# Kernel tuning notes

Hardware: AMD Instinct MI355X
Metric: run time of the kernel (lower is better)

## Reference

```python
import jax, jax.numpy as jnp
import numpy as np


def setup_inputs() -> dict:
    key = jax.random.key(0)
    k1, k2 = jax.random.split(key, 2)
    N, H, W, FIN = 64, 64, 64, 64
    FH, FW, FOUT = 4, 4, 128
    L = (H // FH) * (W // FW)  # 256 output locations (stride == kernel)
    X = jax.random.normal(k1, (N, H, W, FIN), dtype=jnp.float32)
    # 'alexnet' init: normal(0, 0.01), unshared per-location filters
    filters = 0.01 * jax.random.normal(k2, (1, L, FH, FW, FIN, FOUT), dtype=jnp.float32)
    bias = jnp.zeros((FOUT,), dtype=jnp.float32)  # bias init value 0.0
    return {"X": X, "filters": filters, "bias": bias}


def reference(X, filters, bias):
    N, H, W, C = X.shape
    _, L, fh, fw, fin, fout = filters.shape
    rows, cols = H // fh, W // fw
    # image_to_patches (stride==kernel branch): non-overlapping patch extraction
    # patches[n, r*cols+c, i, j, ch] = X[n, r*fh+i, c*fw+j, ch]
    patches = X.reshape(N, rows, fh, cols, fw, C)
    patches = patches.transpose(0, 1, 3, 2, 4, 5).reshape(N, L, fh, fw, C)
    # broadcast-multiply + reduce_sum over (fh, fw, fin) == per-location GEMM
    Z = jnp.einsum('nlijc,lijcf->nlf', patches, filters[0]) + bias
    Z = Z.reshape(N, rows, cols, fout)
    return jax.nn.relu(Z)
```

## Files before the change

kernel.cpp:

```cpp
#include <hip/hip_runtime.h>


typedef __bf16 bf16x8 __attribute__((ext_vector_type(8)));
typedef float f32x4 __attribute__((ext_vector_type(4)));

#define SA 72
#define SB 132

__device__ __forceinline__ unsigned short f2bf(float f) {
  unsigned u = __builtin_bit_cast(unsigned, f);
  u += 0x7fffu + ((u >> 16) & 1u);
  return (unsigned short)(u >> 16);
}
__device__ __forceinline__ unsigned pack2(float a, float b) {
  return (unsigned)f2bf(a) | ((unsigned)f2bf(b) << 16);
}

__global__ __launch_bounds__(256) void bioconv_mfma(
    const float* __restrict__ X, const float* __restrict__ Fw,
    const float* __restrict__ bias, float* __restrict__ out) {
  const int l = blockIdx.x;
  const int r = l >> 4;
  const int c = l & 15;
  const int t = threadIdx.x;
  const int w = t >> 6;
  const int lane = t & 63;
  const int q = lane >> 4;
  const int nl = lane & 15;

  __shared__ __align__(16) unsigned short As[2][64 * SA];
  __shared__ __align__(16) unsigned Bs[2][32 * SB];

  const float* Fl = Fw + (size_t)l * 131072;

  f32x4 acc[4][2];
#pragma unroll
  for (int mb = 0; mb < 4; ++mb)
#pragma unroll
    for (int fb = 0; fb < 2; ++fb)
      acc[mb][fb] = (f32x4){0.f, 0.f, 0.f, 0.f};

  float4 areg[4], b0reg[4], b1reg[4];

  const int a_n0 = t >> 4;
  const int a_f4 = t & 15;
  const int b_kp0 = t >> 5;
  const int b_f = (t & 31) << 2;

  const float* xrowbase = X + c * 256 + a_f4 * 4;

  auto issue_loads = [&](int s) {
    const int i = s >> 2;
    const int koff = (s & 3) << 6;
    const float* xb = xrowbase + (r * 4 + i) * 4096 + koff;
#pragma unroll
    for (int rep = 0; rep < 4; ++rep) {
      const int n = a_n0 + (rep << 4);
      areg[rep] = *(const float4*)(xb + (size_t)n * 262144);
    }
    const float* fbse = Fl + s * 8192 + b_f;
#pragma unroll
    for (int rep = 0; rep < 4; ++rep) {
      const int kp = b_kp0 + (rep << 3);
      const float* g = fbse + kp * 256;
      b0reg[rep] = *(const float4*)(g);
      b1reg[rep] = *(const float4*)(g + 128);
    }
  };

  auto store_lds = [&](int buf) {
#pragma unroll
    for (int rep = 0; rep < 4; ++rep) {
      const int n = a_n0 + (rep << 4);
      uint2 v;
      v.x = pack2(areg[rep].x, areg[rep].y);
      v.y = pack2(areg[rep].z, areg[rep].w);
      *(uint2*)&As[buf][n * SA + a_f4 * 4] = v;
    }
#pragma unroll
    for (int rep = 0; rep < 4; ++rep) {
      const int kp = b_kp0 + (rep << 3);
      uint4 v;
      v.x = pack2(b0reg[rep].x, b1reg[rep].x);
      v.y = pack2(b0reg[rep].y, b1reg[rep].y);
      v.z = pack2(b0reg[rep].z, b1reg[rep].z);
      v.w = pack2(b0reg[rep].w, b1reg[rep].w);
      *(uint4*)&Bs[buf][kp * SB + b_f] = v;
    }
  };

  issue_loads(0);
  store_lds(0);

  for (int s = 0; s < 16; ++s) {
    __syncthreads();
    if (s < 15) issue_loads(s + 1);
    const int buf = s & 1;
#pragma unroll
    for (int kc = 0; kc < 2; ++kc) {
      bf16x8 af[4];
#pragma unroll
      for (int mb = 0; mb < 4; ++mb)
        af[mb] = *(const bf16x8*)&As[buf][(mb * 16 + nl) * SA + kc * 32 + q * 8];
      bf16x8 bfr[2];
#pragma unroll
      for (int fb = 0; fb < 2; ++fb) {
        const unsigned* bp = &Bs[buf][(kc * 16 + q * 4) * SB + (w * 32 + fb * 16 + nl)];
        uint4 v;
        v.x = bp[0];
        v.y = bp[SB];
        v.z = bp[2 * SB];
        v.w = bp[3 * SB];
        bfr[fb] = __builtin_bit_cast(bf16x8, v);
      }
#pragma unroll
      for (int mb = 0; mb < 4; ++mb)
#pragma unroll
        for (int fb = 0; fb < 2; ++fb)
          acc[mb][fb] = __builtin_amdgcn_mfma_f32_16x16x32_bf16(
              af[mb], bfr[fb], acc[mb][fb], 0, 0, 0);
    }
    if (s < 15) store_lds((s + 1) & 1);
  }

#pragma unroll
  for (int fb = 0; fb < 2; ++fb) {
    const int f = w * 32 + fb * 16 + nl;
    const float bv = bias[f];
    float* ob = out + (size_t)l * 128 + f;
#pragma unroll
    for (int mb = 0; mb < 4; ++mb) {
#pragma unroll
      for (int v = 0; v < 4; ++v) {
        const int row = mb * 16 + q * 4 + v;
        const float val = acc[mb][fb][v] + bv;
        ob[(size_t)row * 32768] = fmaxf(val, 0.f);
      }
    }
  }
}

extern "C" void kernel_launch(void* const* d_in, const int* in_sizes, int n_in,
                              void* d_out, int out_size, void* d_ws, size_t ws_size,
                              hipStream_t stream) {
  const float* X = (const float*)d_in[0];
  const float* Fw = (const float*)d_in[1];
  const float* bias = (const float*)d_in[2];
  float* out = (float*)d_out;
  bioconv_mfma<<<256, 256, 0, stream>>>(X, Fw, bias, out);
}
```

Measured before the change: 240.7 us.

## Split output features across four blocks per location to raise occupancy

Each location is now handled by four blocks, one per 32-output-feature slice, giving 1024 blocks instead of 256 on a GPU with 256 CUs. Each wave now owns 16 batch rows across that slice. This spreads the filter streaming, the dominant memory traffic, over more blocks and CUs. The cost is that each block reloads the full X patch tile, so X reads rise fourfold. The bf16 conversion also switches from manual rounding bit math to the compiler's native cast.

```diff
diff --git a/kernel.cpp b/kernel.cpp
--- a/kernel.cpp
+++ b/kernel.cpp
@@ -5,21 +5,21 @@
 typedef float f32x4 __attribute__((ext_vector_type(4)));
 
 #define SA 72
-#define SB 132
+#define SBQ 36
 
-__device__ __forceinline__ unsigned short f2bf(float f) {
-  unsigned u = __builtin_bit_cast(unsigned, f);
-  u += 0x7fffu + ((u >> 16) & 1u);
-  return (unsigned short)(u >> 16);
-}
 __device__ __forceinline__ unsigned pack2(float a, float b) {
-  return (unsigned)f2bf(a) | ((unsigned)f2bf(b) << 16);
+  __bf16 lo = (__bf16)a, hi = (__bf16)b;
+  unsigned short ul = __builtin_bit_cast(unsigned short, lo);
+  unsigned short uh = __builtin_bit_cast(unsigned short, hi);
+  return (unsigned)ul | ((unsigned)uh << 16);
 }
 
 __global__ __launch_bounds__(256) void bioconv_mfma(
     const float* __restrict__ X, const float* __restrict__ Fw,
     const float* __restrict__ bias, float* __restrict__ out) {
-  const int l = blockIdx.x;
+  const int bx = blockIdx.x;
+  const int l = bx & 255;
+  const int fq = bx >> 8;
   const int r = l >> 4;
   const int c = l & 15;
   const int t = threadIdx.x;
@@ -29,23 +29,20 @@
   const int nl = lane & 15;
 
   __shared__ __align__(16) unsigned short As[2][64 * SA];
-  __shared__ __align__(16) unsigned Bs[2][32 * SB];
+  __shared__ __align__(16) unsigned Bs[2][32 * SBQ];
 
-  const float* Fl = Fw + (size_t)l * 131072;
+  const float* Fl = Fw + (size_t)l * 131072 + fq * 32;
 
-  f32x4 acc[4][2];
-#pragma unroll
-  for (int mb = 0; mb < 4; ++mb)
-#pragma unroll
-    for (int fb = 0; fb < 2; ++fb)
-      acc[mb][fb] = (f32x4){0.f, 0.f, 0.f, 0.f};
+  f32x4 acc[2];
+  acc[0] = (f32x4){0.f, 0.f, 0.f, 0.f};
+  acc[1] = (f32x4){0.f, 0.f, 0.f, 0.f};
 
-  float4 areg[4], b0reg[4], b1reg[4];
+  float4 areg[4], b0reg, b1reg;
 
   const int a_n0 = t >> 4;
   const int a_f4 = t & 15;
-  const int b_kp0 = t >> 5;
-  const int b_f = (t & 31) << 2;
+  const int b_kp = t >> 3;
+  const int b_fo = (t & 7) << 2;
 
   const float* xrowbase = X + c * 256 + a_f4 * 4;
 
@@ -58,14 +55,9 @@
       const int n = a_n0 + (rep << 4);
       areg[rep] = *(const float4*)(xb + (size_t)n * 262144);
     }
-    const float* fbse = Fl + s * 8192 + b_f;
-#pragma unroll
-    for (int rep = 0; rep < 4; ++rep) {
-      const int kp = b_kp0 + (rep << 3);
-      const float* g = fbse + kp * 256;
-      b0reg[rep] = *(const float4*)(g);
-      b1reg[rep] = *(const float4*)(g + 128);
-    }
+    const float* g = Fl + s * 8192 + b_kp * 256 + b_fo;
+    b0reg = *(const float4*)(g);
+    b1reg = *(const float4*)(g + 128);
   };
 
   auto store_lds = [&](int buf) {
@@ -77,16 +69,12 @@
       v.y = pack2(areg[rep].z, areg[rep].w);
       *(uint2*)&As[buf][n * SA + a_f4 * 4] = v;
     }
-#pragma unroll
-    for (int rep = 0; rep < 4; ++rep) {
-      const int kp = b_kp0 + (rep << 3);
-      uint4 v;
-      v.x = pack2(b0reg[rep].x, b1reg[rep].x);
-      v.y = pack2(b0reg[rep].y, b1reg[rep].y);
-      v.z = pack2(b0reg[rep].z, b1reg[rep].z);
-      v.w = pack2(b0reg[rep].w, b1reg[rep].w);
-      *(uint4*)&Bs[buf][kp * SB + b_f] = v;
-    }
+    uint4 v;
+    v.x = pack2(b0reg.x, b1reg.x);
+    v.y = pack2(b0reg.y, b1reg.y);
+    v.z = pack2(b0reg.z, b1reg.z);
+    v.w = pack2(b0reg.w, b1reg.w);
+    *(uint4*)&Bs[buf][b_kp * SBQ + b_fo] = v;
   };
 
   issue_loads(0);
@@ -98,44 +86,32 @@
     const int buf = s & 1;
 #pragma unroll
     for (int kc = 0; kc < 2; ++kc) {
-      bf16x8 af[4];
-#pragma unroll
-      for (int mb = 0; mb < 4; ++mb)
-        af[mb] = *(const bf16x8*)&As[buf][(mb * 16 + nl) * SA + kc * 32 + q * 8];
-      bf16x8 bfr[2];
+      bf16x8 af = *(const bf16x8*)&As[buf][(w * 16 + nl) * SA + kc * 32 + q * 8];
 #pragma unroll
       for (int fb = 0; fb < 2; ++fb) {
-        const unsigned* bp = &Bs[buf][(kc * 16 + q * 4) * SB + (w * 32 + fb * 16 + nl)];
+        const unsigned* bp = &Bs[buf][(kc * 16 + q * 4) * SBQ + fb * 16 + nl];
         uint4 v;
         v.x = bp[0];
-        v.y = bp[SB];
-        v.z = bp[2 * SB];
-        v.w = bp[3 * SB];
-        bfr[fb] = __builtin_bit_cast(bf16x8, v);
+        v.y = bp[SBQ];
+        v.z = bp[2 * SBQ];
+        v.w = bp[3 * SBQ];
+        bf16x8 bfr = __builtin_bit_cast(bf16x8, v);
+        acc[fb] = __builtin_amdgcn_mfma_f32_16x16x32_bf16(af, bfr, acc[fb], 0, 0, 0);
       }
-#pragma unroll
-      for (int mb = 0; mb < 4; ++mb)
-#pragma unroll
-        for (int fb = 0; fb < 2; ++fb)
-          acc[mb][fb] = __builtin_amdgcn_mfma_f32_16x16x32_bf16(
-              af[mb], bfr[fb], acc[mb][fb], 0, 0, 0);
     }
     if (s < 15) store_lds((s + 1) & 1);
   }
 
 #pragma unroll
   for (int fb = 0; fb < 2; ++fb) {
-    const int f = w * 32 + fb * 16 + nl;
+    const int f = fq * 32 + fb * 16 + nl;
     const float bv = bias[f];
     float* ob = out + (size_t)l * 128 + f;
 #pragma unroll
-    for (int mb = 0; mb < 4; ++mb) {
-#pragma unroll
-      for (int v = 0; v < 4; ++v) {
-        const int row = mb * 16 + q * 4 + v;
-        const float val = acc[mb][fb][v] + bv;
-        ob[(size_t)row * 32768] = fmaxf(val, 0.f);
-      }
+    for (int v = 0; v < 4; ++v) {
+      const int n = w * 16 + q * 4 + v;
+      const float val = acc[fb][v] + bv;
+      ob[(size_t)n * 32768] = fmaxf(val, 0.f);
     }
   }
 }
@@ -147,5 +123,5 @@
   const float* Fw = (const float*)d_in[1];
   const float* bias = (const float*)d_in[2];
   float* out = (float*)d_out;
-  bioconv_mfma<<<256, 256, 0, stream>>>(X, Fw, bias, out);
+  bioconv_mfma<<<1024, 256, 0, stream>>>(X, Fw, bias, out);
 }
```

Result: no change. 244.9 us (+1.7%).
